# Optimization experiments

Measured on AMD Instinct MI355X. Metric: run time of the kernel, lower is better.

The kernel has to match this reference:

```python
import jax, jax.numpy as jnp
import numpy as np

B, S, HID = 2, 2048, 2048
H, HKV, D = 16, 4, 128        # num_heads, num_kv_heads, head_dim
G = H // HKV                   # GQA group size
CLIP = 8.0                     # clip_qkv
THETA = 10000.0                # rope_theta_within_seq
N_SEQS = 8                     # max_num_sequences


def setup_inputs() -> dict:
    key = jax.random.key(0)
    ks = jax.random.split(key, 6)
    hidden_states = jax.random.normal(ks[0], (B, S, HID), dtype=jnp.float32)
    within_seq_position_ids = jnp.broadcast_to(jnp.arange(S, dtype=jnp.int64), (B, S))
    global_position_ids = jnp.broadcast_to(jnp.arange(S, dtype=jnp.int64), (B, S))
    sequence_ids = jnp.sort(jax.random.randint(ks[1], (B, S), 0, N_SEQS, dtype=jnp.int64), axis=-1)
    scale = 0.02
    Wq = jax.random.normal(ks[2], (H * D, HID), dtype=jnp.float32) * scale
    Wk = jax.random.normal(ks[3], (HKV * D, HID), dtype=jnp.float32) * scale
    Wv = jax.random.normal(ks[4], (HKV * D, HID), dtype=jnp.float32) * scale
    Wo = jax.random.normal(ks[5], (HID, H * D), dtype=jnp.float32) * scale
    return {"hidden_states": hidden_states,
            "within_seq_position_ids": within_seq_position_ids,
            "global_position_ids": global_position_ids,
            "sequence_ids": sequence_ids,
            "Wq": Wq, "Wk": Wk, "Wv": Wv, "Wo": Wo}


def _rotate_half(x):
    x1, x2 = jnp.split(x, 2, axis=-1)
    return jnp.concatenate((-x2, x1), axis=-1)


def _rope_cos_sin(position_ids, dtype):
    # inv_freq: [D/2]
    inv_freq = THETA ** (-(jnp.arange(0, D, 2, dtype=jnp.float32) / D))
    angles = position_ids.astype(jnp.float32)[..., None] * inv_freq  # [B,S,D/2]
    angles = jnp.concatenate((angles, angles), axis=-1)              # [B,S,D]
    # unsqueeze head dim -> [B,S,1,D]
    return jnp.cos(angles)[:, :, None, :].astype(dtype), jnp.sin(angles)[:, :, None, :].astype(dtype)


def reference(hidden_states, within_seq_position_ids, global_position_ids, sequence_ids, Wq, Wk, Wv, Wo):
    b, s, _ = hidden_states.shape
    q = (hidden_states @ Wq.T).reshape(b, s, H, D)
    k = (hidden_states @ Wk.T).reshape(b, s, HKV, D)
    v = (hidden_states @ Wv.T).reshape(b, s, HKV, D)
    # clip_qkv
    q = jnp.clip(q, -CLIP, CLIP)
    k = jnp.clip(k, -CLIP, CLIP)
    v = jnp.clip(v, -CLIP, CLIP)
    # RoPE (within_seq layer -> within_seq_position_ids)
    cos, sin = _rope_cos_sin(within_seq_position_ids, q.dtype)
    q = q * cos + _rotate_half(q) * sin
    k = k * cos + _rotate_half(k) * sin
    # GQA: group queries by kv head instead of materializing repeat_kv
    q = q.transpose(0, 2, 1, 3).reshape(b, HKV, G, s, D)  # [B,HKV,G,S,D]
    k = k.transpose(0, 2, 1, 3)                            # [B,HKV,S,D]
    v = v.transpose(0, 2, 1, 3)
    scores = jnp.einsum('bhgqd,bhkd->bhgqk', q, k) / jnp.sqrt(jnp.asarray(D, q.dtype))
    # block-diagonal (same sequence) causal mask
    qi = jnp.arange(s)
    causal = qi[:, None] >= qi[None, :]                    # [S,S]
    same_seq = sequence_ids[:, :, None] == sequence_ids[:, None, :]  # [B,S,S]
    mask = (causal[None] & same_seq)[:, None, None, :, :]  # [B,1,1,S,S]
    scores = jnp.where(mask, scores, jnp.finfo(scores.dtype).min)
    attn = jax.nn.softmax(scores, axis=-1)
    out = jnp.einsum('bhgqk,bhkd->bhgqd', attn, v)         # [B,HKV,G,S,D]
    out = out.reshape(b, H, s, D).transpose(0, 2, 1, 3).reshape(b, s, H * D)
    return out @ Wo.T
```

## Files before the change

kernel.cpp:

```cpp
#include <hip/hip_runtime.h>
#include <hip/hip_bf16.h>

typedef __hip_bfloat16 bf16;
typedef __attribute__((ext_vector_type(8))) short bf16x8;
typedef __attribute__((ext_vector_type(4))) float f32x4;

#define MFMA_BF16(a, b, c) __builtin_amdgcn_mfma_f32_16x16x32_bf16((a), (b), (c), 0, 0, 0)

#define B_   2
#define S_   2048
#define HID_ 2048
#define H_   16
#define HKV_ 4
#define D_   128

#define GLOAD_LDS(gptr, lptr) \
  __builtin_amdgcn_global_load_lds((const __attribute__((address_space(1))) void*)(gptr), \
                                   (__attribute__((address_space(3))) void*)(lptr), 16, 0, 0)

template <int N>
__device__ __forceinline__ void vmw() {
  if constexpr (N == 0)      asm volatile("s_waitcnt vmcnt(0)" ::: "memory");
  else if constexpr (N == 4) asm volatile("s_waitcnt vmcnt(4)" ::: "memory");
  else if constexpr (N == 5) asm volatile("s_waitcnt vmcnt(5)" ::: "memory");
  else                       asm volatile("s_waitcnt vmcnt(6)" ::: "memory");
}

__device__ __forceinline__ void blk_barrier() {
  __builtin_amdgcn_sched_barrier(0);
  __builtin_amdgcn_s_barrier();
  __builtin_amdgcn_sched_barrier(0);
}

__global__ void cvt_all(const float* __restrict__ hidden, const float* __restrict__ Wq,
                        const float* __restrict__ Wk, const float* __restrict__ Wv,
                        const float* __restrict__ Wo,
                        bf16* __restrict__ Xb, bf16* __restrict__ Wqkv, bf16* __restrict__ Wob) {
  long long i4 = (long long)blockIdx.x * 256 + threadIdx.x;
  const float* src; bf16* dst; long long off;
  if (i4 < 2097152)      { src = hidden; dst = Xb;             off = i4; }
  else if (i4 < 3145728) { src = Wq;     dst = Wqkv;           off = i4 - 2097152; }
  else if (i4 < 3407872) { src = Wk;     dst = Wqkv + 4194304; off = i4 - 3145728; }
  else if (i4 < 3670016) { src = Wv;     dst = Wqkv + 5242880; off = i4 - 3407872; }
  else                   { src = Wo;     dst = Wob;            off = i4 - 3670016; }
  float4 v = *reinterpret_cast<const float4*>(src + off * 4);
  alignas(8) bf16 t[4];
  t[0] = __float2bfloat16(v.x);
  t[1] = __float2bfloat16(v.y);
  t[2] = __float2bfloat16(v.z);
  t[3] = __float2bfloat16(v.w);
  *reinterpret_cast<short4*>(dst + off * 4) = *reinterpret_cast<const short4*>(t);
}

__global__ void seq_start(const int* __restrict__ seq, int* __restrict__ sstart) {
  int t = blockIdx.x * 256 + threadIdx.x;
  int b = t >> 11, s = t & (S_ - 1);
  const int* sb = seq + b * S_;
  int sid = sb[s];
  int lo = 0, hi = s;
  while (lo < hi) {
    int mid = (lo + hi) >> 1;
    if (sb[mid] < sid) lo = mid + 1; else hi = mid;
  }
  sstart[t] = lo;
}

template <int BM, int BN, int OUT_BF16>
__global__ __launch_bounds__(512, 2) void gemm8p(const bf16* __restrict__ A,
                                                 const bf16* __restrict__ Bw,
                                                 void* __restrict__ Cout,
                                                 int M, int N, int K) {
  constexpr int MR = BM / 32;
  constexpr int NR = BN / 64;
  constexpr int LA = BM / 128;
  constexpr int QD = NR + 2;

  __shared__ bf16 As[2][2][BM * 32];
  __shared__ bf16 Bs[2][BN * 64];

  const int tid  = threadIdx.x;
  const int lane = tid & 63;
  const int w    = tid >> 6;
  const int wr   = w >> 2;
  const int wc   = w & 3;
  const int ln15 = lane & 15, g = lane >> 4;

  const int nwg = gridDim.x;
  int bid = blockIdx.x;
  bid = (bid & 7) * (nwg >> 3) + (bid >> 3);
  const int nbn = N / BN;
  const int m0 = (bid / nbn) * BM;
  const int n0 = (bid % nbn) * BN;

  f32x4 acc[MR][NR] = {};

  auto stageA = [&](int db, int kh, int t) {
    int kc = t * 64 + kh * 32;
#pragma unroll
    for (int r = 0; r < LA; r++) {
      int sIdx = r * 512 + tid;
      int row = sIdx >> 2;
      int ss = (sIdx & 3) ^ ((row >> 1) & 3);
      GLOAD_LDS(A + (size_t)(m0 + row) * K + kc + ss * 8, &As[db][kh][(r * 512 + w * 64) * 8]);
    }
  };
  auto stageB = [&](int db, int t) {
#pragma unroll
    for (int r = 0; r < NR; r++) {
      int sIdx = r * 512 + tid;
      int row = sIdx >> 3;
      int cs = (sIdx & 7) ^ (row & 7);
      GLOAD_LDS(Bw + (size_t)(n0 + row) * K + t * 64 + cs * 8, &Bs[db][(size_t)(r * 512 + w * 64) * 8]);
    }
  };

  bf16x8 af[4], bfr[NR];
  auto rdA = [&](int db, int kh, int mb) {
#pragma unroll
    for (int m = 0; m < 4; m++) {
      int row = wr * (BM / 2) + (mb + m) * 16 + ln15;
      af[m] = *reinterpret_cast<const bf16x8*>(&As[db][kh][row * 32 + ((g ^ ((row >> 1) & 3)) << 3)]);
    }
  };
  auto rdB = [&](int db, int kh) {
#pragma unroll
    for (int n = 0; n < NR; n++) {
      int row = wc * (BN / 4) + n * 16 + ln15;
      int sl = ((kh << 2) + g) ^ (row & 7);
      bfr[n] = *reinterpret_cast<const bf16x8*>(&Bs[db][row * 64 + sl * 8]);
    }
  };
  auto MF = [&](int mb) {
    __builtin_amdgcn_s_setprio(1);
#pragma unroll
    for (int m = 0; m < 4; m++)
#pragma unroll
      for (int n = 0; n < NR; n++)
        acc[mb + m][n] = MFMA_BF16(af[m], bfr[n], acc[mb + m][n]);
    __builtin_amdgcn_s_setprio(0);
  };

  const int NT = K >> 6;

  stageA(0, 0, 0);
  stageA(0, 1, 0);
  stageB(0, 0);
  stageA(1, 0, 1);
  stageB(1, 1);
  vmw<QD>();
  blk_barrier();

  for (int T = 0; T < NT; ++T) {
    const int db = T & 1, dn = db ^ 1;

    rdA(db, 0, 0); rdB(db, 0);
    if (T + 1 < NT) stageA(dn, 1, T + 1);
    blk_barrier(); MF(0); blk_barrier();

    rdA(db, 0, 4);
    blk_barrier(); MF(4); blk_barrier();

    rdA(db, 1, 0); rdB(db, 1);
    if (T + 2 < NT) stageA(db, 0, T + 2);
    blk_barrier(); MF(0); blk_barrier();

    rdA(db, 1, 4);
    if (T + 2 < NT) stageB(db, T + 2);
    if (T + 1 < NT) {
      if (T == NT - 2) vmw<0>(); else vmw<QD>();
    }
    blk_barrier(); MF(4); blk_barrier();
  }

#pragma unroll
  for (int m = 0; m < MR; m++)
#pragma unroll
    for (int n = 0; n < NR; n++)
#pragma unroll
      for (int r = 0; r < 4; r++) {
        int row = m0 + wr * (BM / 2) + m * 16 + g * 4 + r;
        int col = n0 + wc * (BN / 4) + n * 16 + ln15;
        if constexpr (OUT_BF16) {
          ((bf16*)Cout)[(size_t)row * N + col] = __float2bfloat16(acc[m][n][r]);
        } else {
          ((float*)Cout)[(size_t)row * N + col] = acc[m][n][r];
        }
      }
}

__global__ __launch_bounds__(256) void qkv_post(const bf16* __restrict__ QKV,
                                                const int* __restrict__ wpos,
                                                bf16* __restrict__ Qs,
                                                bf16* __restrict__ Ks,
                                                bf16* __restrict__ Vt) {
  const int row = blockIdx.x;
  const int b = row >> 11, s = row & (S_ - 1);
  const int t = threadIdx.x;
  const bf16* R = QKV + (size_t)row * 3072;
  const float pos = (float)wpos[row];
  const float kln = 0.14391156831212787f;
  const float qscale = 0.08838834764831845f;

  for (int p = t; p < 1024; p += 256) {
    int h = p >> 6, i = p & 63;
    float ang = pos * expf(-(float)i * kln);
    float sn, cs;
    sincosf(ang, &sn, &cs);
    float x1 = __bfloat162float(R[h * 128 + i]);
    float x2 = __bfloat162float(R[h * 128 + 64 + i]);
    x1 = fminf(fmaxf(x1, -8.f), 8.f);
    x2 = fminf(fmaxf(x2, -8.f), 8.f);
    float y1 = (x1 * cs - x2 * sn) * qscale;
    float y2 = (x2 * cs + x1 * sn) * qscale;
    size_t qb = ((size_t)(b * H_ + h) * S_ + s) * D_;
    Qs[qb + i]      = __float2bfloat16(y1);
    Qs[qb + 64 + i] = __float2bfloat16(y2);
  }
  {
    int kh = t >> 6, i = t & 63;
    float ang = pos * expf(-(float)i * kln);
    float sn, cs;
    sincosf(ang, &sn, &cs);
    float x1 = __bfloat162float(R[2048 + kh * 128 + i]);
    float x2 = __bfloat162float(R[2048 + kh * 128 + 64 + i]);
    x1 = fminf(fmaxf(x1, -8.f), 8.f);
    x2 = fminf(fmaxf(x2, -8.f), 8.f);
    float y1 = x1 * cs - x2 * sn;
    float y2 = x2 * cs + x1 * sn;
    size_t kb = ((size_t)(b * HKV_ + kh) * S_ + s) * D_;
    Ks[kb + i]      = __float2bfloat16(y1);
    Ks[kb + 64 + i] = __float2bfloat16(y2);
  }
  for (int e = t; e < 512; e += 256) {
    int kh = e >> 7, d = e & 127;
    float x = __bfloat162float(R[2560 + e]);
    x = fminf(fmaxf(x, -8.f), 8.f);
    Vt[((size_t)(b * HKV_ + kh) * D_ + d) * S_ + s] = __float2bfloat16(x);
  }
}

__global__ __launch_bounds__(256) void attn_fwd(const bf16* __restrict__ Qs,
                                                const bf16* __restrict__ Ks,
                                                const bf16* __restrict__ Vt,
                                                const int* __restrict__ sstart,
                                                bf16* __restrict__ att) {
  __shared__ bf16 Kl[2][32 * 128];
  __shared__ bf16 Vl[2][128 * 32];
  __shared__ bf16 Plds[4][2][16 * 32];

  const int tid = threadIdx.x;
  const int lane = tid & 63, w = tid >> 6;
  const int ln15 = lane & 15, g = lane >> 4;

  const int wg = ((blockIdx.x & 7) << 6) | (blockIdx.x >> 3);
  const int qt  = wg & 63;
  const int kvh = (wg >> 6) & 3;
  const int b   = wg >> 8;
  const int h   = kvh * 4 + w;
  const int q0  = qt * 32;
  const int qa  = q0 + ln15;
  const int qb  = q0 + 16 + ln15;

  const bf16* Qbase = Qs + (size_t)(b * H_ + h) * S_ * D_;
  bf16x8 qfa[4], qfb[4];
#pragma unroll
  for (int c = 0; c < 4; c++) {
    qfa[c] = *reinterpret_cast<const bf16x8*>(Qbase + (size_t)qa * D_ + c * 32 + g * 8);
    qfb[c] = *reinterpret_cast<const bf16x8*>(Qbase + (size_t)qb * D_ + c * 32 + g * 8);
  }

  const int sQa = sstart[b * S_ + qa];
  const int sQb = sstart[b * S_ + qb];
  const int kstart = __builtin_amdgcn_readfirstlane(__shfl(sQa, 0));
  const int kend = q0 + 31;

  const bf16* Kb = Ks + (size_t)(b * HKV_ + kvh) * S_ * D_;
  const bf16* Vb = Vt + (size_t)(b * HKV_ + kvh) * D_ * S_;

  auto stage = [&](int buf, int kb) {
#pragma unroll
    for (int p = 0; p < 2; p++) {
      int slot = p * 256 + tid;
      int row = slot >> 4;
      int cs = (slot & 15) ^ (row & 15);
      int gr = min(kb + row, S_ - 1);
      GLOAD_LDS(Kb + (size_t)gr * D_ + cs * 8, &Kl[buf][(p * 256 + w * 64) * 8]);
    }
#pragma unroll
    for (int p = 0; p < 2; p++) {
      int slot = p * 256 + tid;
      int d = slot >> 2, c = slot & 3;
      int cs = c ^ (d & 3);
      int gcol = min(kb + cs * 8, S_ - 8);
      GLOAD_LDS(Vb + (size_t)d * S_ + gcol, &Vl[buf][(p * 256 + w * 64) * 8]);
    }
  };

  float ma = -1e30f, la = 0.f, mb = -1e30f, lb = 0.f;
  f32x4 oa[8] = {}, ob[8] = {};

  auto softmax = [&](const f32x4& s0, const f32x4& s1, int qi, int sQ, int kb,
                     float& m, float& lsum, f32x4 (&o)[8], bf16* pdst) {
    float sc[8];
    float tmax = -1e30f;
#pragma unroll
    for (int r = 0; r < 4; r++) {
      int k0i = kb + g * 4 + r;
      int k1i = k0i + 16;
      float x0 = (k0i >= sQ && k0i <= qi) ? s0[r] : -1e30f;
      float x1 = (k1i >= sQ && k1i <= qi) ? s1[r] : -1e30f;
      sc[r] = x0;
      sc[4 + r] = x1;
      tmax = fmaxf(tmax, fmaxf(x0, x1));
    }
    tmax = fmaxf(tmax, __shfl_xor(tmax, 16));
    tmax = fmaxf(tmax, __shfl_xor(tmax, 32));
    float mn  = fmaxf(m, tmax);
    float fac = __expf(m - mn);
    float ps = 0.f;
    alignas(16) bf16 pb[8];
#pragma unroll
    for (int i2 = 0; i2 < 8; i2++) {
      float p = (sc[i2] < -1e29f) ? 0.f : __expf(sc[i2] - mn);
      ps += p;
      pb[i2] = __float2bfloat16(p);
    }
    ps += __shfl_xor(ps, 16);
    ps += __shfl_xor(ps, 32);
    lsum = lsum * fac + ps;
    m = mn;
#pragma unroll
    for (int t2 = 0; t2 < 8; t2++) o[t2] *= fac;
    *reinterpret_cast<short4*>(pdst + ln15 * 32 + g * 4)      = *reinterpret_cast<const short4*>(&pb[0]);
    *reinterpret_cast<short4*>(pdst + ln15 * 32 + 16 + g * 4) = *reinterpret_cast<const short4*>(&pb[4]);
  };

  stage(0, kstart);
  int buf = 0;
  for (int kb = kstart; kb <= kend; kb += 32) {
    __syncthreads();
    if (kb + 32 <= kend) stage(buf ^ 1, kb + 32);

    bf16x8 kf0[4], kf1[4];
#pragma unroll
    for (int c = 0; c < 4; c++) {
      kf0[c] = *reinterpret_cast<const bf16x8*>(&Kl[buf][ln15 * 128 + (((c * 4 + g) ^ ln15) << 3)]);
      kf1[c] = *reinterpret_cast<const bf16x8*>(&Kl[buf][(16 + ln15) * 128 + (((c * 4 + g) ^ ln15) << 3)]);
    }
    f32x4 sa0 = {0.f, 0.f, 0.f, 0.f}, sa1 = sa0, sb0 = sa0, sb1 = sa0;
#pragma unroll
    for (int c = 0; c < 4; c++) {
      sa0 = MFMA_BF16(kf0[c], qfa[c], sa0);
      sa1 = MFMA_BF16(kf1[c], qfa[c], sa1);
      sb0 = MFMA_BF16(kf0[c], qfb[c], sb0);
      sb1 = MFMA_BF16(kf1[c], qfb[c], sb1);
    }

    softmax(sa0, sa1, qa, sQa, kb, ma, la, oa, &Plds[w][0][0]);
    softmax(sb0, sb1, qb, sQb, kb, mb, lb, ob, &Plds[w][1][0]);
    __builtin_amdgcn_wave_barrier();
    bf16x8 pfa = *reinterpret_cast<const bf16x8*>(&Plds[w][0][ln15 * 32 + g * 8]);
    bf16x8 pfb = *reinterpret_cast<const bf16x8*>(&Plds[w][1][ln15 * 32 + g * 8]);

#pragma unroll
    for (int t2 = 0; t2 < 8; t2++) {
      int d = t2 * 16 + ln15;
      bf16x8 vf = *reinterpret_cast<const bf16x8*>(&Vl[buf][d * 32 + ((g ^ (ln15 & 3)) << 3)]);
      oa[t2] = MFMA_BF16(vf, pfa, oa[t2]);
      ob[t2] = MFMA_BF16(vf, pfb, ob[t2]);
    }
    __builtin_amdgcn_wave_barrier();
    buf ^= 1;
  }

  float inva = 1.f / la;
  float invb = 1.f / lb;
#pragma unroll
  for (int t2 = 0; t2 < 8; t2++)
#pragma unroll
    for (int r = 0; r < 4; r++) {
      int d = t2 * 16 + g * 4 + r;
      att[((size_t)(b * S_ + qa)) * (H_ * D_) + h * D_ + d] = __float2bfloat16(oa[t2][r] * inva);
      att[((size_t)(b * S_ + qb)) * (H_ * D_) + h * D_ + d] = __float2bfloat16(ob[t2][r] * invb);
    }
}

extern "C" void kernel_launch(void* const* d_in, const int* in_sizes, int n_in,
                              void* d_out, int out_size, void* d_ws, size_t ws_size,
                              hipStream_t stream) {
  const float* hidden = (const float*)d_in[0];
  const int* wpos = (const int*)d_in[1];
  const int* seq = (const int*)d_in[3];
  const float* Wq = (const float*)d_in[4];
  const float* Wk = (const float*)d_in[5];
  const float* Wv = (const float*)d_in[6];
  const float* Wo = (const float*)d_in[7];

  char* ws = (char*)d_ws;
  bf16* Xb   = (bf16*)(ws);
  bf16* Wqkv = (bf16*)(ws + 16777216);
  bf16* Wob  = (bf16*)(ws + 29360128);
  bf16* QKVb = (bf16*)(ws + 37748736);
  bf16* Ksb  = (bf16*)(ws + 62914560);
  bf16* Vtb  = (bf16*)(ws + 67108864);
  int*  sst  = (int*)(ws + 71303168);
  bf16* Qsb  = Xb;
  bf16* attb = QKVb;

  cvt_all<<<dim3(18432), dim3(256), 0, stream>>>(hidden, Wq, Wk, Wv, Wo, Xb, Wqkv, Wob);
  seq_start<<<dim3(32), dim3(256), 0, stream>>>(seq, sst);

  gemm8p<256, 192, 1><<<dim3(256), dim3(512), 0, stream>>>(Xb, Wqkv, (void*)QKVb, 4096, 3072, 2048);

  qkv_post<<<dim3(4096), dim3(256), 0, stream>>>(QKVb, wpos, Qsb, Ksb, Vtb);

  attn_fwd<<<dim3(512), dim3(256), 0, stream>>>(Qsb, Ksb, Vtb, sst, attb);

  gemm8p<256, 128, 0><<<dim3(256), dim3(512), 0, stream>>>(attb, Wob, d_out, 4096, 2048, 2048);
}
```

Before: 175.1 us.

## Trim GEMM mainloop barriers and move V transpose into tiled LDS kernel

The GEMM main loop drops the barrier before each MFMA phase and places the last phase's MFMA before the vmcnt wait, so LDS reads and compute can overlap with fewer block-wide syncs. Separately, the V clip-and-transpose is taken out of qkv_post and given its own kernel, which stages a 64x128 tile in LDS so that Vt is written with vectorized contiguous stores instead of strided scalar ones. The cost is an extra kernel launch. Removing the pre-MFMA barriers relies on the ds_read completion and the double-buffer ordering staying correct; if they do not, the results could be wrong.

```diff
diff --git a/kernel.cpp b/kernel.cpp
--- a/kernel.cpp
+++ b/kernel.cpp
@@ -155,21 +155,22 @@
 
     rdA(db, 0, 0); rdB(db, 0);
     if (T + 1 < NT) stageA(dn, 1, T + 1);
-    blk_barrier(); MF(0); blk_barrier();
+    MF(0); blk_barrier();
 
     rdA(db, 0, 4);
-    blk_barrier(); MF(4); blk_barrier();
+    MF(4); blk_barrier();
 
     rdA(db, 1, 0); rdB(db, 1);
     if (T + 2 < NT) stageA(db, 0, T + 2);
-    blk_barrier(); MF(0); blk_barrier();
+    MF(0); blk_barrier();
 
     rdA(db, 1, 4);
     if (T + 2 < NT) stageB(db, T + 2);
+    MF(4);
     if (T + 1 < NT) {
       if (T == NT - 2) vmw<0>(); else vmw<QD>();
     }
-    blk_barrier(); MF(4); blk_barrier();
+    blk_barrier();
   }
 
 #pragma unroll
@@ -191,8 +192,7 @@
 __global__ __launch_bounds__(256) void qkv_post(const bf16* __restrict__ QKV,
                                                 const int* __restrict__ wpos,
                                                 bf16* __restrict__ Qs,
-                                                bf16* __restrict__ Ks,
-                                                bf16* __restrict__ Vt) {
+                                                bf16* __restrict__ Ks) {
   const int row = blockIdx.x;
   const int b = row >> 11, s = row & (S_ - 1);
   const int t = threadIdx.x;
@@ -231,11 +231,43 @@
     Ks[kb + i]      = __float2bfloat16(y1);
     Ks[kb + 64 + i] = __float2bfloat16(y2);
   }
-  for (int e = t; e < 512; e += 256) {
-    int kh = e >> 7, d = e & 127;
-    float x = __bfloat162float(R[2560 + e]);
-    x = fminf(fmaxf(x, -8.f), 8.f);
-    Vt[((size_t)(b * HKV_ + kh) * D_ + d) * S_ + s] = __float2bfloat16(x);
+}
+
+__global__ __launch_bounds__(256) void vt_trans(const bf16* __restrict__ QKV,
+                                                bf16* __restrict__ Vt) {
+  __shared__ bf16 Tl[64][132];
+  const int t = threadIdx.x;
+  const int blk = blockIdx.x;
+  const int st = blk & 31, kvh = (blk >> 5) & 3, b = blk >> 7;
+  const int s0 = st * 64;
+
+#pragma unroll
+  for (int p = 0; p < 8; p++) {
+    int r = p * 8 + (t >> 5);
+    int c = (t & 31) * 4;
+    short4 v = *reinterpret_cast<const short4*>(QKV + (size_t)(b * S_ + s0 + r) * 3072 + 2560 + kvh * 128 + c);
+    alignas(8) bf16 e[4];
+    *reinterpret_cast<short4*>(e) = v;
+#pragma unroll
+    for (int k = 0; k < 4; k++) {
+      float x = __bfloat162float(e[k]);
+      x = fminf(fmaxf(x, -8.f), 8.f);
+      Tl[r][c + k] = __float2bfloat16(x);
+    }
+  }
+  __syncthreads();
+
+  if (t < 128) {
+    const int d = t;
+    bf16* dst = Vt + ((size_t)(b * HKV_ + kvh) * D_ + d) * S_ + s0;
+#pragma unroll
+    for (int j = 0; j < 64; j += 8) {
+      alignas(16) bf16 v[8];
+#pragma unroll
+      for (int k = 0; k < 8; k++) v[k] = Tl[j + k][d];
+      *reinterpret_cast<short4*>(dst + j)     = *reinterpret_cast<const short4*>(&v[0]);
+      *reinterpret_cast<short4*>(dst + j + 4) = *reinterpret_cast<const short4*>(&v[4]);
+    }
   }
 }
 
@@ -412,7 +444,8 @@
 
   gemm8p<256, 192, 1><<<dim3(256), dim3(512), 0, stream>>>(Xb, Wqkv, (void*)QKVb, 4096, 3072, 2048);
 
-  qkv_post<<<dim3(4096), dim3(256), 0, stream>>>(QKVb, wpos, Qsb, Ksb, Vtb);
+  qkv_post<<<dim3(4096), dim3(256), 0, stream>>>(QKVb, wpos, Qsb, Ksb);
+  vt_trans<<<dim3(256), dim3(256), 0, stream>>>(QKVb, Vtb);
 
   attn_fwd<<<dim3(512), dim3(256), 0, stream>>>(Qsb, Ksb, Vtb, sst, attb);
 
```

New measurement: 166.2 us. -5.1%, faster.
